# Kernel optimization log

Measured on AMD Instinct MI355X. Metric: run time of the kernel, lower is better.

## Reference

```python
import jax, jax.numpy as jnp
import numpy as np

NUM_HEADS = 12
HEAD_DIM = 64
HIDDEN = NUM_HEADS * HEAD_DIM  # 768
B, L = 4, 512

def setup_inputs() -> dict:
    key = jax.random.key(0)
    ks = jax.random.split(key, 8)
    s = 0.02
    return {
        "hidden_states": jax.random.normal(ks[0], (B, L, HIDDEN), jnp.float32),
        "relation_embedding_k": jax.random.normal(ks[1], (B, L, L, HEAD_DIM), jnp.float32),
        "relation_embedding_v": jax.random.normal(ks[2], (B, L, L, HEAD_DIM), jnp.float32),
        "Wq": jax.random.normal(ks[3], (HIDDEN, HIDDEN), jnp.float32) * s,
        "bq": jnp.zeros((HIDDEN,), jnp.float32),
        "Wk": jax.random.normal(ks[4], (HIDDEN, HIDDEN), jnp.float32) * s,
        "bk": jnp.zeros((HIDDEN,), jnp.float32),
        "Wv": jax.random.normal(ks[5], (HIDDEN, HIDDEN), jnp.float32) * s,
        "bv": jnp.zeros((HIDDEN,), jnp.float32),
    }

def _heads(x):
    # [B, L, HIDDEN] -> [B, H, L, D]
    b, l, _ = x.shape
    return x.reshape(b, l, NUM_HEADS, HEAD_DIM).transpose(0, 2, 1, 3)

def reference(hidden_states, relation_embedding_k, relation_embedding_v,
              Wq, bq, Wk, bk, Wv, bv):
    q = _heads(hidden_states @ Wq + bq)  # [B,H,L,D]
    k = _heads(hidden_states @ Wk + bk)
    v = _heads(hidden_states @ Wv + bv)

    # content scores + relation key scores (shared across heads)
    scores = jnp.einsum('bhld,bhmd->bhlm', q, k)
    scores = scores + jnp.einsum('bhld,blrd->bhlr', q, relation_embedding_k)
    scores = scores / np.sqrt(HEAD_DIM).astype(np.float32)

    probs = jax.nn.softmax(scores, axis=-1)  # [B,H,L,L]

    ctx = jnp.einsum('bhlm,bhmd->bhld', probs, v)
    ctx = ctx + jnp.einsum('bhlr,brld->bhld', probs, relation_embedding_v)

    # [B,H,L,D] -> [B,L,HIDDEN]
    b, h, l, d = ctx.shape
    return ctx.transpose(0, 2, 1, 3).reshape(b, l, h * d)
```

## Files before the change

kernel.cpp:

```cpp
#include <hip/hip_runtime.h>
#include <stdint.h>


typedef __attribute__((ext_vector_type(8))) short bf16x8;
typedef __attribute__((ext_vector_type(4))) float f32x4;
typedef __attribute__((ext_vector_type(4))) unsigned int u32x4;

__device__ __forceinline__ unsigned short f2bf(float f) {
  union { float f; unsigned int u; } v; v.f = f;
  unsigned int r = v.u + 0x7fffu + ((v.u >> 16) & 1u);
  return (unsigned short)(r >> 16);
}
__device__ __forceinline__ float bf2f(unsigned short s) {
  union { unsigned int u; float f; } v; v.u = ((unsigned int)s) << 16;
  return v.f;
}

__global__ void k_cvt_hidden(const float* __restrict__ x, unsigned short* __restrict__ y) {
  int i = blockIdx.x * 256 + threadIdx.x;
  float4 v = reinterpret_cast<const float4*>(x)[i];
  ushort4 o;
  o.x = f2bf(v.x); o.y = f2bf(v.y); o.z = f2bf(v.z); o.w = f2bf(v.w);
  reinterpret_cast<ushort4*>(y)[i] = o;
}

__global__ void k_transp_w(const float* __restrict__ Wq, const float* __restrict__ Wk,
                           const float* __restrict__ Wv, unsigned short* __restrict__ wt) {
  __shared__ float t[64][65];
  const int kt = blockIdx.x, nt = blockIdx.y, wsel = blockIdx.z;
  const float* W = wsel == 0 ? Wq : (wsel == 1 ? Wk : Wv);
  const int lx = threadIdx.x & 63, ly = threadIdx.x >> 6;
  for (int i = 0; i < 64; i += 4)
    t[ly + i][lx] = W[(size_t)(kt * 64 + ly + i) * 768 + nt * 64 + lx];
  __syncthreads();
  for (int i = 0; i < 64; i += 4) {
    int r = ly + i;
    wt[((size_t)wsel * 768 + nt * 64 + r) * 768 + kt * 64 + lx] = f2bf(t[lx][r]);
  }
}

__global__ __launch_bounds__(256) void k_qkv_gemm(
    const unsigned short* __restrict__ A,
    const unsigned short* __restrict__ Bt,
    const float* __restrict__ bq, const float* __restrict__ bk, const float* __restrict__ bv,
    unsigned short* __restrict__ qbf,
    unsigned short* __restrict__ kbf,
    unsigned short* __restrict__ vbt) {
  __shared__ __align__(16) unsigned short lA[64 * 64];
  __shared__ __align__(16) unsigned short lB[64 * 64];
  const int tid = threadIdx.x, lane = tid & 63, w = tid >> 6;
  const int m0 = blockIdx.x * 64, n0 = blockIdx.y * 64;
  const int wm = (w >> 1) * 32, wn = (w & 1) * 32;
  f32x4 acc[2][2] = {};

  for (int kt = 0; kt < 12; ++kt) {
    __syncthreads();
#pragma unroll
    for (int i = 0; i < 2; ++i) {
      int e16 = i * 256 + tid;
      int row = e16 >> 3;
      int kb = (e16 & 7) * 16;
      int dst = row * 128 + (kb ^ ((row & 7) << 4));
      u32x4 va = *(const u32x4*)((const char*)A + (size_t)(m0 + row) * 1536 + kt * 128 + kb);
      *(u32x4*)((char*)lA + dst) = va;
      u32x4 vb = *(const u32x4*)((const char*)Bt + (size_t)(n0 + row) * 1536 + kt * 128 + kb);
      *(u32x4*)((char*)lB + dst) = vb;
    }
    __syncthreads();
#pragma unroll
    for (int ks = 0; ks < 2; ++ks) {
      bf16x8 fa[2], fb[2];
      const int kbyte = (ks * 32 + (lane >> 4) * 8) * 2;
#pragma unroll
      for (int mi = 0; mi < 2; ++mi) {
        int row = wm + mi * 16 + (lane & 15);
        fa[mi] = *(const bf16x8*)((const char*)lA + row * 128 + (kbyte ^ ((row & 7) << 4)));
      }
#pragma unroll
      for (int ni = 0; ni < 2; ++ni) {
        int row = wn + ni * 16 + (lane & 15);
        fb[ni] = *(const bf16x8*)((const char*)lB + row * 128 + (kbyte ^ ((row & 7) << 4)));
      }
#pragma unroll
      for (int mi = 0; mi < 2; ++mi)
#pragma unroll
        for (int ni = 0; ni < 2; ++ni)
          acc[mi][ni] = __builtin_amdgcn_mfma_f32_16x16x32_bf16(fa[mi], fb[ni], acc[mi][ni], 0, 0, 0);
    }
  }
#pragma unroll
  for (int mi = 0; mi < 2; ++mi)
#pragma unroll
    for (int ni = 0; ni < 2; ++ni) {
      int gn = n0 + wn + ni * 16 + (lane & 15);
      float bias = (gn < 768) ? bq[gn] : (gn < 1536 ? bk[gn - 768] : bv[gn - 1536]);
#pragma unroll
      for (int r = 0; r < 4; ++r) {
        int gm = m0 + wm + mi * 16 + ((lane >> 4) << 2) + r;
        float val = acc[mi][ni][r] + bias;
        int b = gm >> 9, l = gm & 511;
        int d = gn & 63;
        if (gn < 768) {
          int h = gn >> 6;
          qbf[(((size_t)(b * 12 + h)) * 512 + l) * 64 + d] = f2bf(val);
        } else if (gn < 1536) {
          int h = (gn - 768) >> 6;
          kbf[(((size_t)(b * 12 + h)) * 512 + l) * 64 + d] = f2bf(val);
        } else {
          int h = (gn - 1536) >> 6;
          vbt[(((size_t)(b * 12 + h)) * 64 + d) * 512 + l] = f2bf(val);
        }
      }
    }
}

__global__ __launch_bounds__(256) void k_scores(
    const unsigned short* __restrict__ qbf, const unsigned short* __restrict__ kbf,
    float* __restrict__ S) {
  __shared__ __align__(16) unsigned short lQ[64 * 64];
  __shared__ __align__(16) unsigned short lK[64 * 64];
  const int tid = threadIdx.x, lane = tid & 63, w = tid >> 6;
  const int mt = blockIdx.x, lt = blockIdx.y, bh = blockIdx.z;
  const int wm = (w >> 1) * 32, wn = (w & 1) * 32;
  f32x4 acc[2][2] = {};
#pragma unroll
  for (int i = 0; i < 2; ++i) {
    int e16 = i * 256 + tid;
    int row = e16 >> 3;
    int kb = (e16 & 7) * 16;
    int dst = row * 128 + (kb ^ ((row & 7) << 4));
    u32x4 vq = *(const u32x4*)((const char*)qbf + ((size_t)bh * 512 + lt * 64 + row) * 128 + kb);
    *(u32x4*)((char*)lQ + dst) = vq;
    u32x4 vk = *(const u32x4*)((const char*)kbf + ((size_t)bh * 512 + mt * 64 + row) * 128 + kb);
    *(u32x4*)((char*)lK + dst) = vk;
  }
  __syncthreads();
#pragma unroll
  for (int ks = 0; ks < 2; ++ks) {
    bf16x8 fa[2], fb[2];
    const int kbyte = (ks * 32 + (lane >> 4) * 8) * 2;
#pragma unroll
    for (int mi = 0; mi < 2; ++mi) {
      int row = wm + mi * 16 + (lane & 15);
      fa[mi] = *(const bf16x8*)((const char*)lQ + row * 128 + (kbyte ^ ((row & 7) << 4)));
    }
#pragma unroll
    for (int ni = 0; ni < 2; ++ni) {
      int row = wn + ni * 16 + (lane & 15);
      fb[ni] = *(const bf16x8*)((const char*)lK + row * 128 + (kbyte ^ ((row & 7) << 4)));
    }
#pragma unroll
    for (int mi = 0; mi < 2; ++mi)
#pragma unroll
      for (int ni = 0; ni < 2; ++ni)
        acc[mi][ni] = __builtin_amdgcn_mfma_f32_16x16x32_bf16(fa[mi], fb[ni], acc[mi][ni], 0, 0, 0);
  }
#pragma unroll
  for (int mi = 0; mi < 2; ++mi)
#pragma unroll
    for (int ni = 0; ni < 2; ++ni) {
      int gm = mt * 64 + wn + ni * 16 + (lane & 15);
#pragma unroll
      for (int r = 0; r < 4; ++r) {
        int gl = lt * 64 + wm + mi * 16 + ((lane >> 4) << 2) + r;
        S[(size_t)bh * 262144 + (size_t)gl * 512 + gm] = acc[mi][ni][r];
      }
    }
}

__global__ __launch_bounds__(256) void k_attn_mid(
    const unsigned short* __restrict__ qbf,
    const float* __restrict__ relk,
    const float* __restrict__ relv,
    const float* __restrict__ S,
    unsigned short* __restrict__ pbf,
    float* __restrict__ crel) {
  __shared__ __align__(16) float qs[12 * 64];
  __shared__ __align__(16) float ps[12 * 512];
  __shared__ __align__(16) float rk[64 * 64];
  const int tid = threadIdx.x, lane = tid & 63, w = tid >> 6;
  const int bl = blockIdx.x;
  const int b = bl >> 9, l = bl & 511;

  for (int i = tid; i < 768; i += 256) {
    int h = i >> 6, d = i & 63;
    qs[i] = bf2f(qbf[(((size_t)(b * 12 + h)) * 512 + l) * 64 + d]);
  }

  float acc[3][8];
#pragma unroll
  for (int hh = 0; hh < 3; ++hh)
#pragma unroll
    for (int j = 0; j < 8; ++j) acc[hh][j] = 0.f;

  const char* relk_base = (const char*)relk + (size_t)bl * 131072;
  for (int t8 = 0; t8 < 8; ++t8) {
    __syncthreads();
#pragma unroll
    for (int i = 0; i < 4; ++i) {
      int e16 = i * 256 + tid;
      int row = e16 >> 4;
      int kb = (e16 & 15) * 16;
      int dst = row * 256 + (kb ^ ((row & 7) << 4));
      u32x4 v = *(const u32x4*)(relk_base + (size_t)t8 * 16384 + (size_t)e16 * 16);
      *(u32x4*)((char*)rk + dst) = v;
    }
    __syncthreads();
#pragma unroll 4
    for (int dc = 0; dc < 16; ++dc) {
      f32x4 rv = *(const f32x4*)((const char*)rk + lane * 256 + ((dc * 16) ^ ((lane & 7) << 4)));
#pragma unroll
      for (int hh = 0; hh < 3; ++hh) {
        f32x4 q4 = *(const f32x4*)&qs[(w * 3 + hh) * 64 + dc * 4];
        acc[hh][t8] += rv.x * q4.x + rv.y * q4.y + rv.z * q4.z + rv.w * q4.w;
      }
    }
  }

#pragma unroll
  for (int hh = 0; hh < 3; ++hh) {
    int h = w * 3 + hh;
    size_t srow = (((size_t)(b * 12 + h)) * 512 + l) * 512;
    float mx = -1e30f;
#pragma unroll
    for (int j = 0; j < 8; ++j) {
      float s = (acc[hh][j] + S[srow + j * 64 + lane]) * 0.125f;
      acc[hh][j] = s;
      mx = fmaxf(mx, s);
    }
#pragma unroll
    for (int off = 32; off; off >>= 1) mx = fmaxf(mx, __shfl_xor(mx, off));
    float sm = 0.f;
#pragma unroll
    for (int j = 0; j < 8; ++j) { acc[hh][j] = __expf(acc[hh][j] - mx); sm += acc[hh][j]; }
#pragma unroll
    for (int off = 32; off; off >>= 1) sm += __shfl_xor(sm, off);
    float inv = 1.f / sm;
#pragma unroll
    for (int j = 0; j < 8; ++j) {
      float pv = acc[hh][j] * inv;
      ps[h * 512 + j * 64 + lane] = pv;
      pbf[srow + j * 64 + lane] = f2bf(pv);
    }
  }
  __syncthreads();

  float cacc[12];
#pragma unroll
  for (int h = 0; h < 12; ++h) cacc[h] = 0.f;
  for (int rc = 0; rc < 32; ++rc) {
    int r0 = w * 128 + rc * 4;
    float v0 = relv[(((size_t)(b * 512 + r0 + 0)) * 512 + l) * 64 + lane];
    float v1 = relv[(((size_t)(b * 512 + r0 + 1)) * 512 + l) * 64 + lane];
    float v2 = relv[(((size_t)(b * 512 + r0 + 2)) * 512 + l) * 64 + lane];
    float v3 = relv[(((size_t)(b * 512 + r0 + 3)) * 512 + l) * 64 + lane];
#pragma unroll
    for (int h = 0; h < 12; ++h) {
      f32x4 p4 = *(const f32x4*)&ps[h * 512 + r0];
      cacc[h] += p4.x * v0 + p4.y * v1 + p4.z * v2 + p4.w * v3;
    }
  }
  __syncthreads();
  float* red = rk;
#pragma unroll
  for (int h = 0; h < 12; ++h) red[(w * 12 + h) * 64 + lane] = cacc[h];
  __syncthreads();
  for (int i = tid; i < 768; i += 256) {
    int h = i >> 6, d = i & 63;
    float s = red[h * 64 + d] + red[(12 + h) * 64 + d] + red[(24 + h) * 64 + d] + red[(36 + h) * 64 + d];
    crel[(size_t)bl * 768 + i] = s;
  }
}

__global__ __launch_bounds__(256) void k_pv(
    const unsigned short* __restrict__ pbf,
    const unsigned short* __restrict__ vbt,
    const float* __restrict__ crel,
    float* __restrict__ out) {
  __shared__ __align__(16) unsigned short lP[64 * 64];
  __shared__ __align__(16) unsigned short lV[64 * 64];
  const int tid = threadIdx.x, lane = tid & 63, w = tid >> 6;
  const int lt = blockIdx.x, bh = blockIdx.y;
  const int b = bh / 12, h = bh % 12;
  const int wm = (w >> 1) * 32, wn = (w & 1) * 32;
  f32x4 acc[2][2] = {};
  const char* pbase = (const char*)pbf + ((size_t)bh * 512 + lt * 64) * 1024;
  const char* vbase = (const char*)vbt + (size_t)bh * 64 * 1024;
  for (int kt = 0; kt < 8; ++kt) {
    __syncthreads();
#pragma unroll
    for (int i = 0; i < 2; ++i) {
      int e16 = i * 256 + tid;
      int row = e16 >> 3;
      int kb = (e16 & 7) * 16;
      int dst = row * 128 + (kb ^ ((row & 7) << 4));
      u32x4 vp = *(const u32x4*)(pbase + (size_t)row * 1024 + kt * 128 + kb);
      *(u32x4*)((char*)lP + dst) = vp;
      u32x4 vv = *(const u32x4*)(vbase + (size_t)row * 1024 + kt * 128 + kb);
      *(u32x4*)((char*)lV + dst) = vv;
    }
    __syncthreads();
#pragma unroll
    for (int ks = 0; ks < 2; ++ks) {
      bf16x8 fa[2], fb[2];
      const int kbyte = (ks * 32 + (lane >> 4) * 8) * 2;
#pragma unroll
      for (int mi = 0; mi < 2; ++mi) {
        int row = wm + mi * 16 + (lane & 15);
        fa[mi] = *(const bf16x8*)((const char*)lP + row * 128 + (kbyte ^ ((row & 7) << 4)));
      }
#pragma unroll
      for (int ni = 0; ni < 2; ++ni) {
        int row = wn + ni * 16 + (lane & 15);
        fb[ni] = *(const bf16x8*)((const char*)lV + row * 128 + (kbyte ^ ((row & 7) << 4)));
      }
#pragma unroll
      for (int mi = 0; mi < 2; ++mi)
#pragma unroll
        for (int ni = 0; ni < 2; ++ni)
          acc[mi][ni] = __builtin_amdgcn_mfma_f32_16x16x32_bf16(fa[mi], fb[ni], acc[mi][ni], 0, 0, 0);
    }
  }
#pragma unroll
  for (int mi = 0; mi < 2; ++mi)
#pragma unroll
    for (int ni = 0; ni < 2; ++ni) {
      int gd = wn + ni * 16 + (lane & 15);
#pragma unroll
      for (int r = 0; r < 4; ++r) {
        int gl = lt * 64 + wm + mi * 16 + ((lane >> 4) << 2) + r;
        size_t o = ((size_t)b * 512 + gl) * 768 + h * 64 + gd;
        out[o] = acc[mi][ni][r] + crel[o];
      }
    }
}

extern "C" void kernel_launch(void* const* d_in, const int* in_sizes, int n_in,
                              void* d_out, int out_size, void* d_ws, size_t ws_size,
                              hipStream_t stream) {
  (void)in_sizes; (void)n_in; (void)out_size; (void)ws_size;
  const float* hidden = (const float*)d_in[0];
  const float* relk   = (const float*)d_in[1];
  const float* relv   = (const float*)d_in[2];
  const float* Wq     = (const float*)d_in[3];
  const float* bq     = (const float*)d_in[4];
  const float* Wk     = (const float*)d_in[5];
  const float* bk     = (const float*)d_in[6];
  const float* Wv     = (const float*)d_in[7];
  const float* bv     = (const float*)d_in[8];
  float* out = (float*)d_out;
  char* ws = (char*)d_ws;

  unsigned short* hb  = (unsigned short*)(ws);
  unsigned short* wt  = (unsigned short*)(ws + 3145728);
  unsigned short* qbf = (unsigned short*)(ws + 6684672);
  unsigned short* kbf = (unsigned short*)(ws + 9830400);
  unsigned short* vbt = (unsigned short*)(ws + 12976128);
  float*          S   = (float*)(ws + 16121856);
  unsigned short* pbf = (unsigned short*)(ws + 66453504);
  float*          cr  = (float*)(ws + 91619328);

  k_cvt_hidden<<<1536, 256, 0, stream>>>(hidden, hb);
  k_transp_w<<<dim3(12, 12, 3), 256, 0, stream>>>(Wq, Wk, Wv, wt);
  k_qkv_gemm<<<dim3(32, 36), 256, 0, stream>>>(hb, wt, bq, bk, bv, qbf, kbf, vbt);
  k_scores<<<dim3(8, 8, 48), 256, 0, stream>>>(qbf, kbf, S);
  k_attn_mid<<<2048, 256, 0, stream>>>(qbf, relk, relv, S, pbf, cr);
  k_pv<<<dim3(8, 48), 256, 0, stream>>>(pbf, vbt, cr, out);
}
```

Measured before the change: 201.9 us.

## Split relation attention kernel and load relk tiles directly into LDS

Splits the fused relation-key/softmax/relation-value kernel into two kernels. The first computes scores and softmax and writes bf16 probabilities. The second rereads those bf16 probabilities from global memory to accumulate against relv. The relk tile staging now uses global_load_lds with the XOR swizzle moved to the source address, which skips the register round trip. Splitting frees the 24KB probability LDS buffer and registers, which may raise occupancy, at the cost of an extra launch, an extra read of the probabilities, and bf16-rounded probabilities in the relv product.

```diff
diff --git a/kernel.cpp b/kernel.cpp
--- a/kernel.cpp
+++ b/kernel.cpp
@@ -14,6 +14,10 @@
 __device__ __forceinline__ float bf2f(unsigned short s) {
   union { unsigned int u; float f; } v; v.u = ((unsigned int)s) << 16;
   return v.f;
+}
+__device__ __forceinline__ void gload_lds16(const void* g, void* l) {
+  __builtin_amdgcn_global_load_lds((const __attribute__((address_space(1))) void*)g,
+                                   (__attribute__((address_space(3))) void*)l, 16, 0, 0);
 }
 
 __global__ void k_cvt_hidden(const float* __restrict__ x, unsigned short* __restrict__ y) {
@@ -168,15 +172,12 @@
     }
 }
 
-__global__ __launch_bounds__(256) void k_attn_mid(
+__global__ __launch_bounds__(256) void k_rel1(
     const unsigned short* __restrict__ qbf,
     const float* __restrict__ relk,
-    const float* __restrict__ relv,
     const float* __restrict__ S,
-    unsigned short* __restrict__ pbf,
-    float* __restrict__ crel) {
+    unsigned short* __restrict__ pbf) {
   __shared__ __align__(16) float qs[12 * 64];
-  __shared__ __align__(16) float ps[12 * 512];
   __shared__ __align__(16) float rk[64 * 64];
   const int tid = threadIdx.x, lane = tid & 63, w = tid >> 6;
   const int bl = blockIdx.x;
@@ -194,16 +195,18 @@
     for (int j = 0; j < 8; ++j) acc[hh][j] = 0.f;
 
   const char* relk_base = (const char*)relk + (size_t)bl * 131072;
+#pragma unroll
   for (int t8 = 0; t8 < 8; ++t8) {
     __syncthreads();
-#pragma unroll
-    for (int i = 0; i < 4; ++i) {
-      int e16 = i * 256 + tid;
-      int row = e16 >> 4;
-      int kb = (e16 & 15) * 16;
-      int dst = row * 256 + (kb ^ ((row & 7) << 4));
-      u32x4 v = *(const u32x4*)(relk_base + (size_t)t8 * 16384 + (size_t)e16 * 16);
-      *(u32x4*)((char*)rk + dst) = v;
+    {
+      const char* gbase = relk_base + t8 * 16384;
+#pragma unroll
+      for (int i = 0; i < 4; ++i) {
+        int slot = i * 256 + tid;
+        int row = slot >> 4, x = slot & 15;
+        const void* src = gbase + row * 256 + ((x * 16) ^ ((row & 7) << 4));
+        gload_lds16(src, (char*)rk + (size_t)(i * 256 + w * 64) * 16);
+      }
     }
     __syncthreads();
 #pragma unroll 4
@@ -237,38 +240,48 @@
     for (int off = 32; off; off >>= 1) sm += __shfl_xor(sm, off);
     float inv = 1.f / sm;
 #pragma unroll
-    for (int j = 0; j < 8; ++j) {
-      float pv = acc[hh][j] * inv;
-      ps[h * 512 + j * 64 + lane] = pv;
-      pbf[srow + j * 64 + lane] = f2bf(pv);
-    }
-  }
-  __syncthreads();
-
-  float cacc[12];
-#pragma unroll
-  for (int h = 0; h < 12; ++h) cacc[h] = 0.f;
+    for (int j = 0; j < 8; ++j)
+      pbf[srow + j * 64 + lane] = f2bf(acc[hh][j] * inv);
+  }
+}
+
+__global__ __launch_bounds__(256) void k_rel2(
+    const unsigned short* __restrict__ pbf,
+    const float* __restrict__ relv,
+    float* __restrict__ crel) {
+  __shared__ __align__(16) float red[4][12][64];
+  const int tid = threadIdx.x, lane = tid & 63, w = tid >> 6;
+  const int bl = blockIdx.x;
+  const int b = bl >> 9, l = bl & 511;
+
+  float acc[12];
+#pragma unroll
+  for (int h = 0; h < 12; ++h) acc[h] = 0.f;
+
+  const float* vbase = relv + ((size_t)b * 512 * 512 + (size_t)l) * 64 + lane;
+  const unsigned short* pb0 = pbf + ((size_t)b * 12 * 512 + l) * 512;
+
+#pragma unroll 2
   for (int rc = 0; rc < 32; ++rc) {
     int r0 = w * 128 + rc * 4;
-    float v0 = relv[(((size_t)(b * 512 + r0 + 0)) * 512 + l) * 64 + lane];
-    float v1 = relv[(((size_t)(b * 512 + r0 + 1)) * 512 + l) * 64 + lane];
-    float v2 = relv[(((size_t)(b * 512 + r0 + 2)) * 512 + l) * 64 + lane];
-    float v3 = relv[(((size_t)(b * 512 + r0 + 3)) * 512 + l) * 64 + lane];
+    float v0 = vbase[(size_t)(r0 + 0) * 32768];
+    float v1 = vbase[(size_t)(r0 + 1) * 32768];
+    float v2 = vbase[(size_t)(r0 + 2) * 32768];
+    float v3 = vbase[(size_t)(r0 + 3) * 32768];
 #pragma unroll
     for (int h = 0; h < 12; ++h) {
-      f32x4 p4 = *(const f32x4*)&ps[h * 512 + r0];
-      cacc[h] += p4.x * v0 + p4.y * v1 + p4.z * v2 + p4.w * v3;
-    }
-  }
-  __syncthreads();
-  float* red = rk;
-#pragma unroll
-  for (int h = 0; h < 12; ++h) red[(w * 12 + h) * 64 + lane] = cacc[h];
+      ushort4 p4 = *(const ushort4*)(pb0 + (size_t)h * 262144 + r0);
+      acc[h] += bf2f(p4.x) * v0 + bf2f(p4.y) * v1 + bf2f(p4.z) * v2 + bf2f(p4.w) * v3;
+    }
+  }
+
+#pragma unroll
+  for (int h = 0; h < 12; ++h) red[w][h][lane] = acc[h];
   __syncthreads();
   for (int i = tid; i < 768; i += 256) {
     int h = i >> 6, d = i & 63;
-    float s = red[h * 64 + d] + red[(12 + h) * 64 + d] + red[(24 + h) * 64 + d] + red[(36 + h) * 64 + d];
-    crel[(size_t)bl * 768 + i] = s;
+    crel[(size_t)bl * 768 + i] =
+        red[0][h][d] + red[1][h][d] + red[2][h][d] + red[3][h][d];
   }
 }
 
@@ -364,6 +377,7 @@
   k_transp_w<<<dim3(12, 12, 3), 256, 0, stream>>>(Wq, Wk, Wv, wt);
   k_qkv_gemm<<<dim3(32, 36), 256, 0, stream>>>(hb, wt, bq, bk, bv, qbf, kbf, vbt);
   k_scores<<<dim3(8, 8, 48), 256, 0, stream>>>(qbf, kbf, S);
-  k_attn_mid<<<2048, 256, 0, stream>>>(qbf, relk, relv, S, pbf, cr);
+  k_rel1<<<2048, 256, 0, stream>>>(qbf, relk, S, pbf);
+  k_rel2<<<2048, 256, 0, stream>>>(pbf, relv, cr);
   k_pv<<<dim3(8, 48), 256, 0, stream>>>(pbf, vbt, cr, out);
 }
```

Result: slower. 225.6 us (+11.7%).

## Rewrite relation attention kernel with bf16 MFMA and register-staged double buffering

Applied to the files above, without the earlier changes.

Replaces the scalar FP32 relation-key dot products and relation-value accumulation in the middle kernel with bf16 MFMA tiles. Relation embeddings are staged through registers with double-buffered LDS and converted to bf16 on the fly. Probabilities are kept in LDS as bf16, and the occupancy hint is raised to three blocks per CU. The kernel is memory bound on reading the large relation tensors, so the gain depends on better load overlap, and bf16 rounding of the relation embeddings adds precision error.

```diff
diff --git a/kernel.cpp b/kernel.cpp
--- a/kernel.cpp
+++ b/kernel.cpp
@@ -5,6 +5,7 @@
 typedef __attribute__((ext_vector_type(8))) short bf16x8;
 typedef __attribute__((ext_vector_type(4))) float f32x4;
 typedef __attribute__((ext_vector_type(4))) unsigned int u32x4;
+typedef __attribute__((ext_vector_type(2))) unsigned int u32x2;
 
 __device__ __forceinline__ unsigned short f2bf(float f) {
   union { float f; unsigned int u; } v; v.f = f;
@@ -14,6 +15,9 @@
 __device__ __forceinline__ float bf2f(unsigned short s) {
   union { unsigned int u; float f; } v; v.u = ((unsigned int)s) << 16;
   return v.f;
+}
+__device__ __forceinline__ void lds_barrier() {
+  asm volatile("s_waitcnt lgkmcnt(0)\ns_barrier" ::: "memory");
 }
 
 __global__ void k_cvt_hidden(const float* __restrict__ x, unsigned short* __restrict__ y) {
@@ -40,11 +44,9 @@
 }
 
 __global__ __launch_bounds__(256) void k_qkv_gemm(
-    const unsigned short* __restrict__ A,
-    const unsigned short* __restrict__ Bt,
+    const unsigned short* __restrict__ A, const unsigned short* __restrict__ Bt,
     const float* __restrict__ bq, const float* __restrict__ bk, const float* __restrict__ bv,
-    unsigned short* __restrict__ qbf,
-    unsigned short* __restrict__ kbf,
+    unsigned short* __restrict__ qbf, unsigned short* __restrict__ kbf,
     unsigned short* __restrict__ vbt) {
   __shared__ __align__(16) unsigned short lA[64 * 64];
   __shared__ __align__(16) unsigned short lB[64 * 64];
@@ -168,115 +170,176 @@
     }
 }
 
-__global__ __launch_bounds__(256) void k_attn_mid(
+__global__ __launch_bounds__(256, 3) void k_rel(
     const unsigned short* __restrict__ qbf,
     const float* __restrict__ relk,
     const float* __restrict__ relv,
     const float* __restrict__ S,
     unsigned short* __restrict__ pbf,
     float* __restrict__ crel) {
-  __shared__ __align__(16) float qs[12 * 64];
-  __shared__ __align__(16) float ps[12 * 512];
-  __shared__ __align__(16) float rk[64 * 64];
+  __shared__ __align__(16) char X[32768];
+  __shared__ __align__(16) unsigned short ps[16 * 512];
   const int tid = threadIdx.x, lane = tid & 63, w = tid >> 6;
-  const int bl = blockIdx.x;
-  const int b = bl >> 9, l = bl & 511;
-
-  for (int i = tid; i < 768; i += 256) {
-    int h = i >> 6, d = i & 63;
-    qs[i] = bf2f(qbf[(((size_t)(b * 12 + h)) * 512 + l) * 64 + d]);
-  }
-
-  float acc[3][8];
-#pragma unroll
-  for (int hh = 0; hh < 3; ++hh)
-#pragma unroll
-    for (int j = 0; j < 8; ++j) acc[hh][j] = 0.f;
-
-  const char* relk_base = (const char*)relk + (size_t)bl * 131072;
-  for (int t8 = 0; t8 < 8; ++t8) {
-    __syncthreads();
-#pragma unroll
-    for (int i = 0; i < 4; ++i) {
-      int e16 = i * 256 + tid;
-      int row = e16 >> 4;
-      int kb = (e16 & 15) * 16;
-      int dst = row * 256 + (kb ^ ((row & 7) << 4));
-      u32x4 v = *(const u32x4*)(relk_base + (size_t)t8 * 16384 + (size_t)e16 * 16);
-      *(u32x4*)((char*)rk + dst) = v;
-    }
-    __syncthreads();
-#pragma unroll 4
-    for (int dc = 0; dc < 16; ++dc) {
-      f32x4 rv = *(const f32x4*)((const char*)rk + lane * 256 + ((dc * 16) ^ ((lane & 7) << 4)));
-#pragma unroll
-      for (int hh = 0; hh < 3; ++hh) {
-        f32x4 q4 = *(const f32x4*)&qs[(w * 3 + hh) * 64 + dc * 4];
-        acc[hh][t8] += rv.x * q4.x + rv.y * q4.y + rv.z * q4.z + rv.w * q4.w;
-      }
-    }
-  }
-
+  const int bl = blockIdx.x, b = bl >> 9, l = bl & 511;
+  const int lm = lane & 15, lg = lane >> 4;
+  const int rr = tid >> 4, xc = tid & 15;
+
+  {
+    u32x4 zz = {0u, 0u, 0u, 0u};
+    *(u32x4*)((char*)ps + 12288 + tid * 16) = zz;
+  }
+
+  const int hq = lm < 12 ? lm : 11;
+  const char* qrow = (const char*)qbf + (((size_t)b * 12 + hq) * 512 + l) * 128;
+  const bf16x8 qa0 = *(const bf16x8*)(qrow + lg * 16);
+  const bf16x8 qa1 = *(const bf16x8*)(qrow + 64 + lg * 16);
+
+  const char* rkbase = (const char*)relk + (size_t)bl * 131072;
+  const char* rvbase = (const char*)relv + (size_t)b * 67108864 + (size_t)l * 256;
+
+  f32x4 stg[2][8];
+  f32x4 accA[4][2];
+#pragma unroll
+  for (int t = 0; t < 4; ++t) {
+    accA[t][0] = {0.f, 0.f, 0.f, 0.f};
+    accA[t][1] = {0.f, 0.f, 0.f, 0.f};
+  }
+
+#pragma unroll
+  for (int i = 0; i < 8; ++i)
+    stg[0][i] = *(const f32x4*)(rkbase + (size_t)(i * 16 + rr) * 256 + xc * 16);
+
+#pragma unroll
+  for (int t = 0; t < 4; ++t) {
+    if (t < 3) {
+#pragma unroll
+      for (int i = 0; i < 8; ++i)
+        stg[(t + 1) & 1][i] =
+            *(const f32x4*)(rkbase + (size_t)((t + 1) * 128 + i * 16 + rr) * 256 + xc * 16);
+    }
+    char* buf = X + (t & 1) * 16384;
+#pragma unroll
+    for (int i = 0; i < 8; ++i) {
+      const int rl = i * 16 + rr;
+      f32x4 v = stg[t & 1][i];
+      u32x2 pk;
+      pk.x = (unsigned)f2bf(v[0]) | ((unsigned)f2bf(v[1]) << 16);
+      pk.y = (unsigned)f2bf(v[2]) | ((unsigned)f2bf(v[3]) << 16);
+      *(u32x2*)(buf + rl * 128 + ((xc * 8) ^ ((rl & 7) << 4))) = pk;
+    }
+    lds_barrier();
+#pragma unroll
+    for (int p = 0; p < 2; ++p) {
+      const int rrow = (w * 2 + p) * 16 + lm;
+      const char* base = buf + rrow * 128;
+      bf16x8 fb0 = *(const bf16x8*)(base + ((lg * 16) ^ ((rrow & 7) << 4)));
+      bf16x8 fb1 = *(const bf16x8*)(base + ((64 + lg * 16) ^ ((rrow & 7) << 4)));
+      accA[t][p] = __builtin_amdgcn_mfma_f32_16x16x32_bf16(qa0, fb0, accA[t][p], 0, 0, 0);
+      accA[t][p] = __builtin_amdgcn_mfma_f32_16x16x32_bf16(qa1, fb1, accA[t][p], 0, 0, 0);
+    }
+  }
+
+  float sreg[3][8];
 #pragma unroll
   for (int hh = 0; hh < 3; ++hh) {
-    int h = w * 3 + hh;
-    size_t srow = (((size_t)(b * 12 + h)) * 512 + l) * 512;
+    const float* sp = S + (((size_t)b * 12 + (w * 3 + hh)) * 512 + l) * 512 + lane;
+#pragma unroll
+    for (int j = 0; j < 8; ++j) sreg[hh][j] = sp[j * 64];
+  }
+
+  lds_barrier();
+  if (lg < 3) {
+#pragma unroll
+    for (int t = 0; t < 4; ++t)
+#pragma unroll
+      for (int p = 0; p < 2; ++p) {
+        const int r = t * 128 + w * 32 + p * 16 + lm;
+#pragma unroll
+        for (int reg = 0; reg < 4; ++reg) {
+          const int h = lg * 4 + reg;
+          *(float*)(X + h * 2048 + ((r * 4) ^ ((h & 7) << 4))) = accA[t][p][reg];
+        }
+      }
+  }
+  lds_barrier();
+
+#pragma unroll
+  for (int i = 0; i < 8; ++i)
+    stg[0][i] = *(const f32x4*)(rvbase + (size_t)(i * 16 + rr) * 131072 + xc * 16);
+
+#pragma unroll
+  for (int hh = 0; hh < 3; ++hh) {
+    const int h = w * 3 + hh;
+    const size_t srow = (((size_t)b * 12 + h) * 512 + l) * 512;
+    float sv[8];
     float mx = -1e30f;
 #pragma unroll
     for (int j = 0; j < 8; ++j) {
-      float s = (acc[hh][j] + S[srow + j * 64 + lane]) * 0.125f;
-      acc[hh][j] = s;
+      const int r = j * 64 + lane;
+      float sr = *(const float*)(X + h * 2048 + ((r * 4) ^ ((h & 7) << 4)));
+      float s = (sr + sreg[hh][j]) * 0.125f;
+      sv[j] = s;
       mx = fmaxf(mx, s);
     }
 #pragma unroll
     for (int off = 32; off; off >>= 1) mx = fmaxf(mx, __shfl_xor(mx, off));
     float sm = 0.f;
 #pragma unroll
-    for (int j = 0; j < 8; ++j) { acc[hh][j] = __expf(acc[hh][j] - mx); sm += acc[hh][j]; }
+    for (int j = 0; j < 8; ++j) { sv[j] = __expf(sv[j] - mx); sm += sv[j]; }
 #pragma unroll
     for (int off = 32; off; off >>= 1) sm += __shfl_xor(sm, off);
-    float inv = 1.f / sm;
+    const float inv = 1.f / sm;
 #pragma unroll
     for (int j = 0; j < 8; ++j) {
-      float pv = acc[hh][j] * inv;
-      ps[h * 512 + j * 64 + lane] = pv;
-      pbf[srow + j * 64 + lane] = f2bf(pv);
-    }
-  }
-  __syncthreads();
-
-  float cacc[12];
-#pragma unroll
-  for (int h = 0; h < 12; ++h) cacc[h] = 0.f;
-  for (int rc = 0; rc < 32; ++rc) {
-    int r0 = w * 128 + rc * 4;
-    float v0 = relv[(((size_t)(b * 512 + r0 + 0)) * 512 + l) * 64 + lane];
-    float v1 = relv[(((size_t)(b * 512 + r0 + 1)) * 512 + l) * 64 + lane];
-    float v2 = relv[(((size_t)(b * 512 + r0 + 2)) * 512 + l) * 64 + lane];
-    float v3 = relv[(((size_t)(b * 512 + r0 + 3)) * 512 + l) * 64 + lane];
-#pragma unroll
-    for (int h = 0; h < 12; ++h) {
-      f32x4 p4 = *(const f32x4*)&ps[h * 512 + r0];
-      cacc[h] += p4.x * v0 + p4.y * v1 + p4.z * v2 + p4.w * v3;
-    }
-  }
-  __syncthreads();
-  float* red = rk;
-#pragma unroll
-  for (int h = 0; h < 12; ++h) red[(w * 12 + h) * 64 + lane] = cacc[h];
-  __syncthreads();
-  for (int i = tid; i < 768; i += 256) {
-    int h = i >> 6, d = i & 63;
-    float s = red[h * 64 + d] + red[(12 + h) * 64 + d] + red[(24 + h) * 64 + d] + red[(36 + h) * 64 + d];
-    crel[(size_t)bl * 768 + i] = s;
+      const int r = j * 64 + lane;
+      const unsigned short pb = f2bf(sv[j] * inv);
+      *(unsigned short*)((char*)ps + h * 1024 + ((r * 2) ^ ((h & 7) << 4))) = pb;
+      pbf[srow + r] = pb;
+    }
+  }
+  lds_barrier();
+
+  f32x4 accC = {0.f, 0.f, 0.f, 0.f};
+#pragma unroll
+  for (int t = 0; t < 4; ++t) {
+    if (t < 3) {
+#pragma unroll
+      for (int i = 0; i < 8; ++i)
+        stg[(t + 1) & 1][i] =
+            *(const f32x4*)(rvbase + (size_t)((t + 1) * 128 + i * 16 + rr) * 131072 + xc * 16);
+    }
+    char* buf = X + (t & 1) * 16384;
+#pragma unroll
+    for (int i = 0; i < 8; ++i) {
+      const int rl = i * 16 + rr;
+      f32x4 v = stg[t & 1][i];
+#pragma unroll
+      for (int e = 0; e < 4; ++e) {
+        const int d = xc * 4 + e;
+        *(unsigned short*)(buf + d * 256 + ((rl * 2) ^ ((d & 15) << 4))) = f2bf(v[e]);
+      }
+    }
+    lds_barrier();
+    const int drow = w * 16 + lm;
+    const char* abase = buf + drow * 256;
+#pragma unroll
+    for (int kk = 0; kk < 4; ++kk) {
+      bf16x8 fa = *(const bf16x8*)(abase + (((kk * 32 + lg * 8) * 2) ^ ((drow & 15) << 4)));
+      const int rg = t * 128 + kk * 32 + lg * 8;
+      bf16x8 fp = *(const bf16x8*)((const char*)ps + lm * 1024 + ((rg * 2) ^ ((lm & 7) << 4)));
+      accC = __builtin_amdgcn_mfma_f32_16x16x32_bf16(fa, fp, accC, 0, 0, 0);
+    }
+  }
+  if (lm < 12) {
+#pragma unroll
+    for (int reg = 0; reg < 4; ++reg)
+      crel[(size_t)bl * 768 + lm * 64 + w * 16 + lg * 4 + reg] = accC[reg];
   }
 }
 
 __global__ __launch_bounds__(256) void k_pv(
-    const unsigned short* __restrict__ pbf,
-    const unsigned short* __restrict__ vbt,
-    const float* __restrict__ crel,
-    float* __restrict__ out) {
+    const unsigned short* __restrict__ pbf, const unsigned short* __restrict__ vbt,
+    const float* __restrict__ crel, float* __restrict__ out) {
   __shared__ __align__(16) unsigned short lP[64 * 64];
   __shared__ __align__(16) unsigned short lV[64 * 64];
   const int tid = threadIdx.x, lane = tid & 63, w = tid >> 6;
@@ -364,6 +427,6 @@
   k_transp_w<<<dim3(12, 12, 3), 256, 0, stream>>>(Wq, Wk, Wv, wt);
   k_qkv_gemm<<<dim3(32, 36), 256, 0, stream>>>(hb, wt, bq, bk, bv, qbf, kbf, vbt);
   k_scores<<<dim3(8, 8, 48), 256, 0, stream>>>(qbf, kbf, S);
-  k_attn_mid<<<2048, 256, 0, stream>>>(qbf, relk, relv, S, pbf, cr);
+  k_rel<<<2048, 256, 0, stream>>>(qbf, relk, relv, S, pbf, cr);
   k_pv<<<dim3(8, 48), 256, 0, stream>>>(pbf, vbt, cr, out);
 }
```

After: 189.1 us. 1.07x faster.
